# Performance work log

Hardware: AMD Instinct MI355X
Metric: run time of the kernel (lower is better)

The kernel has to match this reference:

```python
import jax, jax.numpy as jnp
import numpy as np

B, L, H = 16384, 4096, 1024

def setup_inputs() -> dict:
    key = jax.random.key(0)
    k1, k2, k3, k4 = jax.random.split(key, 4)
    return {
        "bert_output": jax.random.normal(k1, (B, H), dtype=jnp.float32),
        "label_embed": jax.random.normal(k2, (L, H), dtype=jnp.float32),
        "W": jax.random.normal(k3, (L, H), dtype=jnp.float32) * (1.0 / np.sqrt(H)),
        "b": jax.random.normal(k4, (L,), dtype=jnp.float32) * 0.02,
    }

def reference(bert_output, label_embed, W, b):
    # Faithful fused form of the original double loop:
    #   logits[i, j] = (W @ (bert_output[i] + label_embed[j]) + b)[j]
    #               = W[j] . bert_output[i] + W[j] . label_embed[j] + b[j]
    # [B,H] @ [H,L] -> [B,L]
    cross = jnp.einsum('bh,lh->bl', bert_output, W)
    # per-label diagonal term: W[j] . label_embed[j]  -> [L]
    label_bias = jnp.einsum('lh,lh->l', W, label_embed) + b
    logits = cross + label_bias[None, :]
    return logits
```

## Files before the change

### kernel.cpp

```cpp
#include <hip/hip_runtime.h>
#include <hip/hip_bf16.h>

constexpr int BDIM = 16384;
constexpr int LDIM = 4096;
constexpr int HDIM = 1024;

constexpr int BM = 256;
constexpr int BN = 128;
constexpr int BK = 64;
constexpr int KTILES = HDIM / BK;

typedef __attribute__((ext_vector_type(4))) int i32x4;

__global__ void prep_kernel(const float* __restrict__ A, const float* __restrict__ W,
                            const float* __restrict__ E, const float* __restrict__ b,
                            signed char* __restrict__ Aq, signed char* __restrict__ Wq,
                            float* __restrict__ sA, float* __restrict__ sW,
                            float* __restrict__ bias) {
  const int bid = blockIdx.x;
  const int w = threadIdx.x >> 6;
  const int l = threadIdx.x & 63;
  const bool isW = bid < (LDIM / 4);
  const int row = isW ? bid * 4 + w : (bid - LDIM / 4) * 4 + w;
  const float4* s4 = (const float4*)((isW ? W : A) + (size_t)row * HDIM);

  float4 v[4];
  float amax = 0.f, dot = 0.f;
#pragma unroll
  for (int i = 0; i < 4; ++i) {
    v[i] = s4[i * 64 + l];
    amax = fmaxf(amax, fmaxf(fmaxf(fabsf(v[i].x), fabsf(v[i].y)),
                             fmaxf(fabsf(v[i].z), fabsf(v[i].w))));
  }
  if (isW) {
    const float4* e4 = (const float4*)(E + (size_t)row * HDIM);
#pragma unroll
    for (int i = 0; i < 4; ++i) {
      float4 ev = e4[i * 64 + l];
      dot += v[i].x * ev.x + v[i].y * ev.y + v[i].z * ev.z + v[i].w * ev.w;
    }
  }
#pragma unroll
  for (int o = 32; o > 0; o >>= 1) amax = fmaxf(amax, __shfl_xor(amax, o, 64));
  if (isW) {
#pragma unroll
    for (int o = 32; o > 0; o >>= 1) dot += __shfl_xor(dot, o, 64);
  }
  const float inv = amax > 0.f ? 127.f / amax : 0.f;
  unsigned int* dst = (unsigned int*)((isW ? Wq : Aq) + (size_t)row * HDIM);
#pragma unroll
  for (int i = 0; i < 4; ++i) {
    int q0 = (int)rintf(v[i].x * inv), q1 = (int)rintf(v[i].y * inv);
    int q2 = (int)rintf(v[i].z * inv), q3 = (int)rintf(v[i].w * inv);
    dst[i * 64 + l] =
        (q0 & 255) | ((q1 & 255) << 8) | ((q2 & 255) << 16) | ((q3 & 255) << 24);
  }
  if (l == 0) {
    if (isW) { sW[row] = amax * (1.f / 127.f); bias[row] = dot + b[row]; }
    else sA[row] = amax * (1.f / 127.f);
  }
}

__device__ __forceinline__ void gld_lds16(const void* g, void* l) {
  __builtin_amdgcn_global_load_lds(
      (const __attribute__((address_space(1))) void*)g,
      (__attribute__((address_space(3))) void*)l, 16, 0, 0);
}

#define MEMPIN asm volatile("" ::: "memory")
#define SCHED0 __builtin_amdgcn_sched_barrier(0)
#define BAR __builtin_amdgcn_s_barrier()
#define LGKM0 asm volatile("s_waitcnt lgkmcnt(0)" ::: "memory")
#define VM3 asm volatile("s_waitcnt vmcnt(3)" ::: "memory")
#define VM0 asm volatile("s_waitcnt vmcnt(0)" ::: "memory")
#define VMNONE (void)0

__global__ __launch_bounds__(512, 4) void gemm_kernel(
    const signed char* __restrict__ Aq,
    const signed char* __restrict__ Wq,
    const float* __restrict__ sA,
    const float* __restrict__ sW,
    const float* __restrict__ bias,
    float* __restrict__ C)
{
  __shared__ __attribute__((aligned(128))) signed char As[3 * BM * BK];
  __shared__ __attribute__((aligned(128))) signed char Bs[3 * BN * BK];

  const int tid = threadIdx.x;
  const int w = tid >> 6;
  const int l = tid & 63;
  const int wr = w >> 1;
  const int wc = w & 1;
  const int lr = l & 15;
  const int hi = l >> 4;

  const int bid = blockIdx.x;
  const int swz = (bid & 7) * 256 + (bid >> 3);
  const int mblk = swz >> 5;
  const int nblk = swz & 31;
  const int brow = mblk * BM;
  const int bcol = nblk * BN;

  const int srow = tid >> 2;
  const int scn = (tid & 3) ^ ((tid >> 3) & 3);
  const signed char* aSrc = Aq + (size_t)(brow + srow) * HDIM + scn * 16;
  const signed char* bSrc = Wq + (size_t)(bcol + srow) * HDIM + scn * 16;

  const int c0 = (hi ^ ((lr >> 1) & 3)) * 16;
  const int rowA = wr * 64 + lr;
  const int rowB = wc * 64 + lr;

  i32x4 acc[4][4] = {};
  i32x4 aF[4], bF[4];

#define ISSUE_A(s, kk)                                                         \
  { const signed char* s_ = aSrc + (kk) * BK;                                  \
    gld_lds16(s_, &As[(s) * 16384 + w * 1024]);                                \
    gld_lds16(s_ + (size_t)128 * HDIM, &As[(s) * 16384 + 8192 + w * 1024]); }
#define ISSUE_B(s, kk)                                                         \
  gld_lds16(bSrc + (kk) * BK, &Bs[(s) * 8192 + w * 1024]);

#define READ_AB(s)                                                             \
  _Pragma("unroll") for (int mi = 0; mi < 4; ++mi)                             \
    aF[mi] = *(const i32x4*)&As[(s) * 16384 + (rowA + mi * 16) * 64 + c0];     \
  _Pragma("unroll") for (int ni = 0; ni < 4; ++ni)                             \
    bF[ni] = *(const i32x4*)&Bs[(s) * 8192 + (rowB + ni * 16) * 64 + c0];

#define MFMA16                                                                 \
  _Pragma("unroll") for (int mi = 0; mi < 4; ++mi) {                           \
    _Pragma("unroll") for (int ni = 0; ni < 4; ++ni) {                         \
      acc[mi][ni] = __builtin_amdgcn_mfma_i32_16x16x64_i8(                     \
          aF[mi], bF[ni], acc[mi][ni], 0, 0, 0);                               \
    }                                                                          \
  }

#define TILE(s, s2, SS, tk2, VMW, DOBAR)                                       \
  { READ_AB(s)                                                                 \
    if (SS) { ISSUE_A((s2), (tk2)); ISSUE_B((s2), (tk2)); }                    \
    SCHED0; LGKM0; SCHED0;                                                     \
    __builtin_amdgcn_s_setprio(1);                                             \
    MFMA16                                                                     \
    __builtin_amdgcn_s_setprio(0);                                             \
    SCHED0;                                                                    \
    VMW; MEMPIN;                                                               \
    if (DOBAR) BAR;                                                            \
    MEMPIN; }

  ISSUE_A(0, 0); ISSUE_B(0, 0); ISSUE_A(1, 1); ISSUE_B(1, 1);
  VM3;
  MEMPIN; BAR;

#pragma unroll 1
  for (int t = 0; t < 12; t += 3) {
    TILE(0, 2, 1, t + 2, VM3, 1);
    TILE(1, 0, 1, t + 3, VM3, 1);
    TILE(2, 1, 1, t + 4, VM3, 1);
  }
  TILE(0, 2, 1, 14, VM3, 1);
  TILE(1, 0, 1, 15, VM3, 1);
  TILE(2, 0, 0, 0, VM0, 1);
  TILE(0, 0, 0, 0, VMNONE, 0);

  float sw4[4], bv[4];
#pragma unroll
  for (int ni = 0; ni < 4; ++ni) {
    const int cc = bcol + wc * 64 + ni * 16 + lr;
    sw4[ni] = sW[cc];
    bv[ni] = bias[cc];
  }
  const int orow0 = brow + wr * 64 + hi * 4;
  const int ocol0 = bcol + wc * 64 + lr;
#pragma unroll
  for (int mi = 0; mi < 4; ++mi) {
#pragma unroll
    for (int r = 0; r < 4; ++r) {
      const float sa = sA[orow0 + mi * 16 + r];
#pragma unroll
      for (int ni = 0; ni < 4; ++ni) {
        C[(size_t)(orow0 + mi * 16 + r) * LDIM + ocol0 + ni * 16] =
            (float)acc[mi][ni][r] * (sa * sw4[ni]) + bv[ni];
      }
    }
  }
#undef TILE
#undef MFMA16
#undef READ_AB
#undef ISSUE_A
#undef ISSUE_B
}

extern "C" void kernel_launch(void* const* d_in, const int* in_sizes, int n_in,
                              void* d_out, int out_size, void* d_ws, size_t ws_size,
                              hipStream_t stream) {
  const float* bert = (const float*)d_in[0];
  const float* emb  = (const float*)d_in[1];
  const float* W    = (const float*)d_in[2];
  const float* b    = (const float*)d_in[3];
  float* out = (float*)d_out;

  char* ws = (char*)d_ws;
  signed char* Aq = (signed char*)ws;
  signed char* Wq = (signed char*)(ws + (size_t)BDIM * HDIM);
  float* sAp  = (float*)(ws + (size_t)BDIM * HDIM + (size_t)LDIM * HDIM);
  float* sWp  = (float*)((char*)sAp + BDIM * sizeof(float));
  float* bias = (float*)((char*)sWp + LDIM * sizeof(float));

  hipLaunchKernelGGL(prep_kernel, dim3(LDIM / 4 + BDIM / 4), dim3(256), 0, stream,
                     bert, W, emb, b, Aq, Wq, sAp, sWp, bias);
  hipLaunchKernelGGL(gemm_kernel, dim3((BDIM / BM) * (LDIM / BN)), dim3(512), 0, stream,
                     Aq, Wq, sAp, sWp, bias, out);
}
```

Before: 136.5 us.

## Shrink GEMM tile to 128x128 with 4 waves and double buffering

Cuts the int8 GEMM block tile from 256x128 with 8 waves to 128x128 with 4 waves. The shared-memory pipeline drops from three stages to two, with a full vmcnt(0) wait and a barrier per K tile, and the MFMA priority bumps are removed. The block-index swizzle is changed to group M blocks per XCD. Smaller blocks and less LDS per block raise occupancy and grid count, but data reuse per block falls and the shallower pipeline exposes more load latency.

Result: slower. 149.5 us (+9.6%).

```diff
diff --git a/kernel.cpp b/kernel.cpp
--- a/kernel.cpp
+++ b/kernel.cpp
@@ -5,7 +5,7 @@
 constexpr int LDIM = 4096;
 constexpr int HDIM = 1024;
 
-constexpr int BM = 256;
+constexpr int BM = 128;
 constexpr int BN = 128;
 constexpr int BK = 64;
 constexpr int KTILES = HDIM / BK;
@@ -71,11 +71,9 @@
 #define SCHED0 __builtin_amdgcn_sched_barrier(0)
 #define BAR __builtin_amdgcn_s_barrier()
 #define LGKM0 asm volatile("s_waitcnt lgkmcnt(0)" ::: "memory")
-#define VM3 asm volatile("s_waitcnt vmcnt(3)" ::: "memory")
 #define VM0 asm volatile("s_waitcnt vmcnt(0)" ::: "memory")
-#define VMNONE (void)0
-
-__global__ __launch_bounds__(512, 4) void gemm_kernel(
+
+__global__ __launch_bounds__(256, 4) void gemm_kernel(
     const signed char* __restrict__ Aq,
     const signed char* __restrict__ Wq,
     const float* __restrict__ sA,
@@ -83,8 +81,8 @@
     const float* __restrict__ bias,
     float* __restrict__ C)
 {
-  __shared__ __attribute__((aligned(128))) signed char As[3 * BM * BK];
-  __shared__ __attribute__((aligned(128))) signed char Bs[3 * BN * BK];
+  __shared__ __attribute__((aligned(128))) signed char As[2 * BM * BK];
+  __shared__ __attribute__((aligned(128))) signed char Bs[2 * BN * BK];
 
   const int tid = threadIdx.x;
   const int w = tid >> 6;
@@ -95,9 +93,9 @@
   const int hi = l >> 4;
 
   const int bid = blockIdx.x;
-  const int swz = (bid & 7) * 256 + (bid >> 3);
-  const int mblk = swz >> 5;
-  const int nblk = swz & 31;
+  const int idx = bid >> 3;
+  const int mblk = (bid & 7) * 16 + (idx & 15);
+  const int nblk = idx >> 4;
   const int brow = mblk * BM;
   const int bcol = nblk * BN;
 
@@ -113,18 +111,19 @@
   i32x4 acc[4][4] = {};
   i32x4 aF[4], bF[4];
 
-#define ISSUE_A(s, kk)                                                         \
-  { const signed char* s_ = aSrc + (kk) * BK;                                  \
-    gld_lds16(s_, &As[(s) * 16384 + w * 1024]);                                \
-    gld_lds16(s_ + (size_t)128 * HDIM, &As[(s) * 16384 + 8192 + w * 1024]); }
-#define ISSUE_B(s, kk)                                                         \
-  gld_lds16(bSrc + (kk) * BK, &Bs[(s) * 8192 + w * 1024]);
-
-#define READ_AB(s)                                                             \
+#define STAGE(d, kk)                                                           \
+  { const signed char* a_ = aSrc + (kk) * BK;                                  \
+    gld_lds16(a_, &As[(d) * 8192 + w * 1024]);                                 \
+    gld_lds16(a_ + (size_t)64 * HDIM, &As[(d) * 8192 + 4096 + w * 1024]);      \
+    const signed char* b_ = bSrc + (kk) * BK;                                  \
+    gld_lds16(b_, &Bs[(d) * 8192 + w * 1024]);                                 \
+    gld_lds16(b_ + (size_t)64 * HDIM, &Bs[(d) * 8192 + 4096 + w * 1024]); }
+
+#define READ_AB(d)                                                             \
   _Pragma("unroll") for (int mi = 0; mi < 4; ++mi)                             \
-    aF[mi] = *(const i32x4*)&As[(s) * 16384 + (rowA + mi * 16) * 64 + c0];     \
+    aF[mi] = *(const i32x4*)&As[(d) * 8192 + (rowA + mi * 16) * 64 + c0];      \
   _Pragma("unroll") for (int ni = 0; ni < 4; ++ni)                             \
-    bF[ni] = *(const i32x4*)&Bs[(s) * 8192 + (rowB + ni * 16) * 64 + c0];
+    bF[ni] = *(const i32x4*)&Bs[(d) * 8192 + (rowB + ni * 16) * 64 + c0];
 
 #define MFMA16                                                                 \
   _Pragma("unroll") for (int mi = 0; mi < 4; ++mi) {                           \
@@ -134,32 +133,25 @@
     }                                                                          \
   }
 
-#define TILE(s, s2, SS, tk2, VMW, DOBAR)                                       \
-  { READ_AB(s)                                                                 \
-    if (SS) { ISSUE_A((s2), (tk2)); ISSUE_B((s2), (tk2)); }                    \
+#define REGION(d, SS, kk1, TAIL)                                               \
+  { if (SS) STAGE((d) ^ 1, (kk1));                                             \
+    READ_AB(d)                                                                 \
     SCHED0; LGKM0; SCHED0;                                                     \
-    __builtin_amdgcn_s_setprio(1);                                             \
     MFMA16                                                                     \
-    __builtin_amdgcn_s_setprio(0);                                             \
     SCHED0;                                                                    \
-    VMW; MEMPIN;                                                               \
-    if (DOBAR) BAR;                                                            \
-    MEMPIN; }
-
-  ISSUE_A(0, 0); ISSUE_B(0, 0); ISSUE_A(1, 1); ISSUE_B(1, 1);
-  VM3;
+    if (!(TAIL)) { VM0; MEMPIN; BAR; MEMPIN; } }
+
+  STAGE(0, 0);
+  VM0;
   MEMPIN; BAR;
 
 #pragma unroll 1
-  for (int t = 0; t < 12; t += 3) {
-    TILE(0, 2, 1, t + 2, VM3, 1);
-    TILE(1, 0, 1, t + 3, VM3, 1);
-    TILE(2, 1, 1, t + 4, VM3, 1);
-  }
-  TILE(0, 2, 1, 14, VM3, 1);
-  TILE(1, 0, 1, 15, VM3, 1);
-  TILE(2, 0, 0, 0, VM0, 1);
-  TILE(0, 0, 0, 0, VMNONE, 0);
+  for (int t = 0; t < KTILES - 2; t += 2) {
+    REGION(0, 1, t + 1, 0);
+    REGION(1, 1, t + 2, 0);
+  }
+  REGION(0, 1, KTILES - 1, 0);
+  REGION(1, 0, 0, 1);
 
   float sw4[4], bv[4];
 #pragma unroll
@@ -182,11 +174,10 @@
       }
     }
   }
-#undef TILE
+#undef REGION
 #undef MFMA16
 #undef READ_AB
-#undef ISSUE_A
-#undef ISSUE_B
+#undef STAGE
 }
 
 extern "C" void kernel_launch(void* const* d_in, const int* in_sizes, int n_in,
@@ -207,6 +198,6 @@
 
   hipLaunchKernelGGL(prep_kernel, dim3(LDIM / 4 + BDIM / 4), dim3(256), 0, stream,
                      bert, W, emb, b, Aq, Wq, sAp, sWp, bias);
-  hipLaunchKernelGGL(gemm_kernel, dim3((BDIM / BM) * (LDIM / BN)), dim3(512), 0, stream,
+  hipLaunchKernelGGL(gemm_kernel, dim3((BDIM / BM) * (LDIM / BN)), dim3(256), 0, stream,
                      Aq, Wq, sAp, sWp, bias, out);
 }
```

## Halve GEMM block to four waves, each computing a 128x64 sub-tile

Applied to the files above, without the earlier changes.

The int8 GEMM block drops from 8 waves to 4 while keeping the 256x128 block tile. Each wave now computes 128x64 with 8x4 MFMA accumulators, so each LDS fragment read feeds more MFMAs. Each thread issues more global-to-LDS loads per stage, and the vmcnt waits are adjusted to match. The cost is higher accumulator register pressure and fewer resident waves per CU to hide latency.

After: 134.1 us. Within noise of the previous version (-1.7%).

```diff
diff --git a/kernel.cpp b/kernel.cpp
--- a/kernel.cpp
+++ b/kernel.cpp
@@ -71,11 +71,11 @@
 #define SCHED0 __builtin_amdgcn_sched_barrier(0)
 #define BAR __builtin_amdgcn_s_barrier()
 #define LGKM0 asm volatile("s_waitcnt lgkmcnt(0)" ::: "memory")
-#define VM3 asm volatile("s_waitcnt vmcnt(3)" ::: "memory")
+#define VM6 asm volatile("s_waitcnt vmcnt(6)" ::: "memory")
 #define VM0 asm volatile("s_waitcnt vmcnt(0)" ::: "memory")
 #define VMNONE (void)0
 
-__global__ __launch_bounds__(512, 4) void gemm_kernel(
+__global__ __launch_bounds__(256, 2) void gemm_kernel(
     const signed char* __restrict__ Aq,
     const signed char* __restrict__ Wq,
     const float* __restrict__ sA,
@@ -107,59 +107,64 @@
   const signed char* bSrc = Wq + (size_t)(bcol + srow) * HDIM + scn * 16;
 
   const int c0 = (hi ^ ((lr >> 1) & 3)) * 16;
-  const int rowA = wr * 64 + lr;
-  const int rowB = wc * 64 + lr;
-
-  i32x4 acc[4][4] = {};
-  i32x4 aF[4], bF[4];
+
+  i32x4 acc[8][4] = {};
+  i32x4 aF[8], bF[4];
 
 #define ISSUE_A(s, kk)                                                         \
   { const signed char* s_ = aSrc + (kk) * BK;                                  \
-    gld_lds16(s_, &As[(s) * 16384 + w * 1024]);                                \
-    gld_lds16(s_ + (size_t)128 * HDIM, &As[(s) * 16384 + 8192 + w * 1024]); }
+    _Pragma("unroll") for (int i = 0; i < 4; ++i)                              \
+      gld_lds16(s_ + (size_t)64 * i * HDIM,                                    \
+                &As[(s) * 16384 + i * 4096 + w * 1024]); }
 #define ISSUE_B(s, kk)                                                         \
-  gld_lds16(bSrc + (kk) * BK, &Bs[(s) * 8192 + w * 1024]);
+  { const signed char* s_ = bSrc + (kk) * BK;                                  \
+    _Pragma("unroll") for (int i = 0; i < 2; ++i)                              \
+      gld_lds16(s_ + (size_t)64 * i * HDIM,                                    \
+                &Bs[(s) * 8192 + i * 4096 + w * 1024]); }
 
 #define READ_AB(s)                                                             \
-  _Pragma("unroll") for (int mi = 0; mi < 4; ++mi)                             \
-    aF[mi] = *(const i32x4*)&As[(s) * 16384 + (rowA + mi * 16) * 64 + c0];     \
+  _Pragma("unroll") for (int mi = 0; mi < 8; ++mi)                             \
+    aF[mi] = *(const i32x4*)&As[(s) * 16384 +                                  \
+                                (wr * 128 + mi * 16 + lr) * 64 + c0];          \
   _Pragma("unroll") for (int ni = 0; ni < 4; ++ni)                             \
-    bF[ni] = *(const i32x4*)&Bs[(s) * 8192 + (rowB + ni * 16) * 64 + c0];
-
-#define MFMA16                                                                 \
-  _Pragma("unroll") for (int mi = 0; mi < 4; ++mi) {                           \
+    bF[ni] = *(const i32x4*)&Bs[(s) * 8192 +                                   \
+                                (wc * 64 + ni * 16 + lr) * 64 + c0];
+
+#define MFMA32                                                                 \
+  _Pragma("unroll") for (int mi = 0; mi < 8; ++mi) {                           \
     _Pragma("unroll") for (int ni = 0; ni < 4; ++ni) {                         \
       acc[mi][ni] = __builtin_amdgcn_mfma_i32_16x16x64_i8(                     \
           aF[mi], bF[ni], acc[mi][ni], 0, 0, 0);                               \
     }                                                                          \
   }
 
-#define TILE(s, s2, SS, tk2, VMW, DOBAR)                                       \
+#define REGION(s, s2, SS, kk2, VMW, DOBAR)                                     \
   { READ_AB(s)                                                                 \
-    if (SS) { ISSUE_A((s2), (tk2)); ISSUE_B((s2), (tk2)); }                    \
+    if (SS) { ISSUE_A((s2), (kk2)); ISSUE_B((s2), (kk2)); }                    \
     SCHED0; LGKM0; SCHED0;                                                     \
     __builtin_amdgcn_s_setprio(1);                                             \
-    MFMA16                                                                     \
+    MFMA32                                                                     \
     __builtin_amdgcn_s_setprio(0);                                             \
     SCHED0;                                                                    \
     VMW; MEMPIN;                                                               \
     if (DOBAR) BAR;                                                            \
     MEMPIN; }
 
-  ISSUE_A(0, 0); ISSUE_B(0, 0); ISSUE_A(1, 1); ISSUE_B(1, 1);
-  VM3;
+  ISSUE_A(0, 0); ISSUE_B(0, 0);
+  ISSUE_A(1, 1); ISSUE_B(1, 1);
+  VM6;
   MEMPIN; BAR;
 
 #pragma unroll 1
   for (int t = 0; t < 12; t += 3) {
-    TILE(0, 2, 1, t + 2, VM3, 1);
-    TILE(1, 0, 1, t + 3, VM3, 1);
-    TILE(2, 1, 1, t + 4, VM3, 1);
-  }
-  TILE(0, 2, 1, 14, VM3, 1);
-  TILE(1, 0, 1, 15, VM3, 1);
-  TILE(2, 0, 0, 0, VM0, 1);
-  TILE(0, 0, 0, 0, VMNONE, 0);
+    REGION(0, 2, 1, t + 2, VM6, 1);
+    REGION(1, 0, 1, t + 3, VM6, 1);
+    REGION(2, 1, 1, t + 4, VM6, 1);
+  }
+  REGION(0, 2, 1, 14, VM6, 1);
+  REGION(1, 0, 1, 15, VM6, 1);
+  REGION(2, 0, 0, 0, VM0, 1);
+  REGION(0, 0, 0, 0, VMNONE, 0);
 
   float sw4[4], bv[4];
 #pragma unroll
@@ -168,10 +173,10 @@
     sw4[ni] = sW[cc];
     bv[ni] = bias[cc];
   }
-  const int orow0 = brow + wr * 64 + hi * 4;
+  const int orow0 = brow + wr * 128 + hi * 4;
   const int ocol0 = bcol + wc * 64 + lr;
 #pragma unroll
-  for (int mi = 0; mi < 4; ++mi) {
+  for (int mi = 0; mi < 8; ++mi) {
 #pragma unroll
     for (int r = 0; r < 4; ++r) {
       const float sa = sA[orow0 + mi * 16 + r];
@@ -182,8 +187,8 @@
       }
     }
   }
-#undef TILE
-#undef MFMA16
+#undef REGION
+#undef MFMA32
 #undef READ_AB
 #undef ISSUE_A
 #undef ISSUE_B
@@ -207,6 +212,6 @@
 
   hipLaunchKernelGGL(prep_kernel, dim3(LDIM / 4 + BDIM / 4), dim3(256), 0, stream,
                      bert, W, emb, b, Aq, Wq, sAp, sWp, bias);
-  hipLaunchKernelGGL(gemm_kernel, dim3((BDIM / BM) * (LDIM / BN)), dim3(512), 0, stream,
+  hipLaunchKernelGGL(gemm_kernel, dim3((BDIM / BM) * (LDIM / BN)), dim3(256), 0, stream,
                      Aq, Wq, sAp, sWp, bias, out);
 }
```
